# Optimization experiments

Measured on AMD Instinct MI355X. Metric: run time of the kernel, lower is better.

Reference implementation:

```python
import jax, jax.numpy as jnp
import numpy as np
from jax import lax

TAU = 20.0
DT = 1.0
THRESH = 1.0

# Hard-threshold spike with surrogate gradient (triangular window around thresh),
# matching torch SpikeFunction.
@jax.custom_vjp
def spike(v):
    return (v >= THRESH).astype(v.dtype)

def _spike_fwd(v):
    return spike(v), v

def _spike_bwd(v, g):
    return (g * jnp.clip(1.0 - jnp.abs(v - THRESH), 0.0, 1.0),)

spike.defvjp(_spike_fwd, _spike_bwd)


def setup_inputs() -> dict:
    key = jax.random.key(0)
    B, F, T = 64, 2048, 512
    x = jax.random.normal(key, (B, F, T), dtype=jnp.float32)
    return {"x": x}


def reference(x) -> jnp.ndarray:
    # x: [B, F, T]; sequential LIF membrane scan over T with spike + hard reset.
    B, F, T = x.shape

    def step(v, x_t):
        v = v + (x_t - v) * (DT / TAU)
        s = spike(v)
        v = v * (1.0 - s)  # reset-to-zero on spike
        return v, s

    x_tmajor = jnp.moveaxis(x, 2, 0)  # [T, B, F]
    v0 = jnp.zeros((B, F), dtype=x.dtype)
    _, spikes = lax.scan(step, v0, x_tmajor)  # spikes: [T, B, F]
    return jnp.moveaxis(spikes, 0, 2)  # [B, F, T]
```

## Files before the change

kernel.cpp:

```cpp
#include <hip/hip_runtime.h>


#define T_LEN 512
#define CHUNK 64
#define ROWS 256
#define NCHUNK (T_LEN / CHUNK)

__global__ __launch_bounds__(256, 2)
void lif_kernel(const float* __restrict__ x, float* __restrict__ out) {
    __shared__ float tile[CHUNK][ROWS];
    const int tid  = threadIdx.x;
    const int row0 = blockIdx.x * ROWS;
    const float k = 1.0f / 20.0f;
    float v = 0.0f;

    for (int ch = 0; ch < NCHUNK; ++ch) {
        const int t0 = ch * CHUNK;

        #pragma unroll
        for (int p = 0; p < 16; ++p) {
            const int q = p * 256 + tid;
            const int r = q >> 4;
            const int c = (q & 15) * 4;
            const float4 val = *reinterpret_cast<const float4*>(
                x + (size_t)(row0 + r) * T_LEN + t0 + c);
            tile[c + 0][r ^ (c + 0)] = val.x;
            tile[c + 1][r ^ (c + 1)] = val.y;
            tile[c + 2][r ^ (c + 2)] = val.z;
            tile[c + 3][r ^ (c + 3)] = val.w;
        }
        __syncthreads();

        #pragma unroll
        for (int t = 0; t < CHUNK; ++t) {
            const float xv = tile[t][tid ^ t];
            v = v + (xv - v) * k;
            const bool fire = (v >= 1.0f);
            tile[t][tid ^ t] = fire ? 1.0f : 0.0f;
            v = fire ? 0.0f : v;
        }
        __syncthreads();

        #pragma unroll
        for (int p = 0; p < 16; ++p) {
            const int q = p * 256 + tid;
            const int r = q >> 4;
            const int c = (q & 15) * 4;
            float4 val;
            val.x = tile[c + 0][r ^ (c + 0)];
            val.y = tile[c + 1][r ^ (c + 1)];
            val.z = tile[c + 2][r ^ (c + 2)];
            val.w = tile[c + 3][r ^ (c + 3)];
            *reinterpret_cast<float4*>(
                out + (size_t)(row0 + r) * T_LEN + t0 + c) = val;
        }
        __syncthreads();
    }
}

extern "C" void kernel_launch(void* const* d_in, const int* in_sizes, int n_in,
                              void* d_out, int out_size, void* d_ws, size_t ws_size,
                              hipStream_t stream) {
    const float* x = (const float*)d_in[0];
    float* out = (float*)d_out;
    const int rows = in_sizes[0] / T_LEN;
    const int grid = rows / ROWS;
    lif_kernel<<<dim3(grid), dim3(ROWS), 0, stream>>>(x, out);
}
```

Before: 441.2 us.

## Use single-wavefront blocks with register double-buffered prefetch of next chunk

Shrinks each block to one 64-lane wavefront handling 64 rows, so the __syncthreads barriers are replaced by LDS waitcnt fences. The next chunk's global loads are issued into a 16-entry float4 register buffer before the current chunk's sequential scan runs, overlapping memory latency with compute. This raises register pressure and quadruples the grid size, and it relies on wavefront-synchronous LDS semantics for correctness.

```diff
diff --git a/kernel.cpp b/kernel.cpp
--- a/kernel.cpp
+++ b/kernel.cpp
@@ -3,58 +3,75 @@
 
 #define T_LEN 512
 #define CHUNK 64
-#define ROWS 256
 #define NCHUNK (T_LEN / CHUNK)
 
-__global__ __launch_bounds__(256, 2)
+__global__ __launch_bounds__(64, 2)
 void lif_kernel(const float* __restrict__ x, float* __restrict__ out) {
-    __shared__ float tile[CHUNK][ROWS];
-    const int tid  = threadIdx.x;
-    const int row0 = blockIdx.x * ROWS;
-    const float k = 1.0f / 20.0f;
+    __shared__ float tile[CHUNK][64];
+    const int lane = threadIdx.x;
+    const size_t row0 = (size_t)blockIdx.x * 64;
+    const float kk = 1.0f / 20.0f;
     float v = 0.0f;
 
+    const float* xb = x + row0 * T_LEN;
+    float* ob = out + row0 * T_LEN;
+
+    const int rL = lane >> 4;
+    const int cL = (lane & 15) * 4;
+
+    float4 buf[16];
+
+    #pragma unroll
+    for (int p = 0; p < 16; ++p) {
+        const int r = p * 4 + rL;
+        buf[p] = *reinterpret_cast<const float4*>(xb + (size_t)r * T_LEN + cL);
+    }
+
     for (int ch = 0; ch < NCHUNK; ++ch) {
-        const int t0 = ch * CHUNK;
-
         #pragma unroll
         for (int p = 0; p < 16; ++p) {
-            const int q = p * 256 + tid;
-            const int r = q >> 4;
-            const int c = (q & 15) * 4;
-            const float4 val = *reinterpret_cast<const float4*>(
-                x + (size_t)(row0 + r) * T_LEN + t0 + c);
-            tile[c + 0][r ^ (c + 0)] = val.x;
-            tile[c + 1][r ^ (c + 1)] = val.y;
-            tile[c + 2][r ^ (c + 2)] = val.z;
-            tile[c + 3][r ^ (c + 3)] = val.w;
+            const int r = p * 4 + rL;
+            tile[cL + 0][r ^ (cL + 0)] = buf[p].x;
+            tile[cL + 1][r ^ (cL + 1)] = buf[p].y;
+            tile[cL + 2][r ^ (cL + 2)] = buf[p].z;
+            tile[cL + 3][r ^ (cL + 3)] = buf[p].w;
         }
-        __syncthreads();
+
+        if (ch + 1 < NCHUNK) {
+            const float* xc = xb + (size_t)(ch + 1) * CHUNK;
+            #pragma unroll
+            for (int p = 0; p < 16; ++p) {
+                const int r = p * 4 + rL;
+                buf[p] = *reinterpret_cast<const float4*>(xc + (size_t)r * T_LEN + cL);
+            }
+        }
+
+        asm volatile("s_waitcnt lgkmcnt(0)" ::: "memory");
 
         #pragma unroll
         for (int t = 0; t < CHUNK; ++t) {
-            const float xv = tile[t][tid ^ t];
-            v = v + (xv - v) * k;
+            const float xv = tile[t][lane ^ t];
+            v = v + (xv - v) * kk;
             const bool fire = (v >= 1.0f);
-            tile[t][tid ^ t] = fire ? 1.0f : 0.0f;
+            tile[t][lane ^ t] = fire ? 1.0f : 0.0f;
             v = fire ? 0.0f : v;
         }
-        __syncthreads();
 
+        asm volatile("s_waitcnt lgkmcnt(0)" ::: "memory");
+
+        float* oc = ob + (size_t)ch * CHUNK;
         #pragma unroll
         for (int p = 0; p < 16; ++p) {
-            const int q = p * 256 + tid;
-            const int r = q >> 4;
-            const int c = (q & 15) * 4;
-            float4 val;
-            val.x = tile[c + 0][r ^ (c + 0)];
-            val.y = tile[c + 1][r ^ (c + 1)];
-            val.z = tile[c + 2][r ^ (c + 2)];
-            val.w = tile[c + 3][r ^ (c + 3)];
-            *reinterpret_cast<float4*>(
-                out + (size_t)(row0 + r) * T_LEN + t0 + c) = val;
+            const int r = p * 4 + rL;
+            float4 s;
+            s.x = tile[cL + 0][r ^ (cL + 0)];
+            s.y = tile[cL + 1][r ^ (cL + 1)];
+            s.z = tile[cL + 2][r ^ (cL + 2)];
+            s.w = tile[cL + 3][r ^ (cL + 3)];
+            *reinterpret_cast<float4*>(oc + (size_t)r * T_LEN + cL) = s;
         }
-        __syncthreads();
+
+        asm volatile("s_waitcnt lgkmcnt(0)" ::: "memory");
     }
 }
 
@@ -64,6 +81,6 @@
     const float* x = (const float*)d_in[0];
     float* out = (float*)d_out;
     const int rows = in_sizes[0] / T_LEN;
-    const int grid = rows / ROWS;
-    lif_kernel<<<dim3(grid), dim3(ROWS), 0, stream>>>(x, out);
+    const int grid = rows / 64;
+    lif_kernel<<<dim3(grid), dim3(64), 0, stream>>>(x, out);
 }
```

Measured after the change: 441.9 us. Within noise of the previous version (+0.2%).

## Replace tiled sequential LIF scan with wave-level parallel prefix and spike-free fast path

Applied to the files above, without the earlier changes.

Each wave handles one row at a time. Each lane holds 8 contiguous timesteps, and the no-reset membrane trajectory is computed with a shuffle-based parallel prefix scan using precomputed decay powers. If no lane's membrane comes near threshold (checked with a ballot against a 0.95 margin), the row is written as zeros directly. Otherwise every lane reruns the exact sequential scan for that row. This drops the shared-memory transpose and the barriers and streams memory more directly, but rows that do spike pay a costly redundant serial fallback.

```diff
diff --git a/kernel.cpp b/kernel.cpp
--- a/kernel.cpp
+++ b/kernel.cpp
@@ -1,60 +1,82 @@
 #include <hip/hip_runtime.h>
 
 
+typedef float f8 __attribute__((ext_vector_type(8)));
+
 #define T_LEN 512
-#define CHUNK 64
-#define ROWS 256
-#define NCHUNK (T_LEN / CHUNK)
+#define ROWS_PER_WAVE 16
+#define WAVES_PER_BLOCK 4
 
-__global__ __launch_bounds__(256, 2)
+__global__ __launch_bounds__(256, 8)
 void lif_kernel(const float* __restrict__ x, float* __restrict__ out) {
-    __shared__ float tile[CHUNK][ROWS];
-    const int tid  = threadIdx.x;
-    const int row0 = blockIdx.x * ROWS;
-    const float k = 1.0f / 20.0f;
-    float v = 0.0f;
+    constexpr float  K  = 1.0f / 20.0f;
+    constexpr double Kd = (double)(1.0f / 20.0f);
+    constexpr double A1 = 1.0 - Kd;
+    constexpr double A2 = A1 * A1;
+    constexpr double A4 = A2 * A2;
+    constexpr double A8 = A4 * A4;
+    constexpr double A16 = A8 * A8;
+    constexpr double A32 = A16 * A16;
+    constexpr double A64 = A32 * A32;
+    constexpr double A128 = A64 * A64;
+    constexpr double A256 = A128 * A128;
+    constexpr float C[6] = {(float)A8,  (float)A16,  (float)A32,
+                            (float)A64, (float)A128, (float)A256};
 
-    for (int ch = 0; ch < NCHUNK; ++ch) {
-        const int t0 = ch * CHUNK;
+    const int lane = threadIdx.x & 63;
+    const int wid  = blockIdx.x * WAVES_PER_BLOCK + (threadIdx.x >> 6);
+    const size_t row0 = (size_t)wid * ROWS_PER_WAVE;
+
+    const f8 zero8 = {0.f, 0.f, 0.f, 0.f, 0.f, 0.f, 0.f, 0.f};
+
+    f8 xv = *(const f8*)(x + row0 * T_LEN + lane * 8);
+
+    for (int rr = 0; rr < ROWS_PER_WAVE; ++rr) {
+        const size_t base = (row0 + rr) * T_LEN;
+        const f8 xc = xv;
+        if (rr + 1 < ROWS_PER_WAVE)
+            xv = *(const f8*)(x + base + T_LEN + lane * 8);
+
+        float b = 0.0f;
+        #pragma unroll
+        for (int j = 0; j < 8; ++j) b = b + (xc[j] - b) * K;
 
         #pragma unroll
-        for (int p = 0; p < 16; ++p) {
-            const int q = p * 256 + tid;
-            const int r = q >> 4;
-            const int c = (q & 15) * 4;
-            const float4 val = *reinterpret_cast<const float4*>(
-                x + (size_t)(row0 + r) * T_LEN + t0 + c);
-            tile[c + 0][r ^ (c + 0)] = val.x;
-            tile[c + 1][r ^ (c + 1)] = val.y;
-            tile[c + 2][r ^ (c + 2)] = val.z;
-            tile[c + 3][r ^ (c + 3)] = val.w;
+        for (int s = 0; s < 6; ++s) {
+            const float o = __shfl_up(b, 1 << s);
+            const float f = fmaf(o, C[s], b);
+            b = (lane >= (1 << s)) ? f : b;
         }
-        __syncthreads();
+        float u = __shfl_up(b, 1);
+        u = (lane == 0) ? 0.0f : u;
 
+        float v = u;
+        float mx = -1.0f;
         #pragma unroll
-        for (int t = 0; t < CHUNK; ++t) {
-            const float xv = tile[t][tid ^ t];
-            v = v + (xv - v) * k;
-            const bool fire = (v >= 1.0f);
-            tile[t][tid ^ t] = fire ? 1.0f : 0.0f;
-            v = fire ? 0.0f : v;
+        for (int j = 0; j < 8; ++j) {
+            v = v + (xc[j] - v) * K;
+            mx = fmaxf(mx, v);
         }
-        __syncthreads();
 
-        #pragma unroll
-        for (int p = 0; p < 16; ++p) {
-            const int q = p * 256 + tid;
-            const int r = q >> 4;
-            const int c = (q & 15) * 4;
-            float4 val;
-            val.x = tile[c + 0][r ^ (c + 0)];
-            val.y = tile[c + 1][r ^ (c + 1)];
-            val.z = tile[c + 2][r ^ (c + 2)];
-            val.w = tile[c + 3][r ^ (c + 3)];
-            *reinterpret_cast<float4*>(
-                out + (size_t)(row0 + r) * T_LEN + t0 + c) = val;
+        if (__builtin_expect(__ballot(mx >= 0.95f) != 0, 0)) {
+            const float* xr = x + base;
+            unsigned m = 0;
+            float vv = 0.0f;
+            for (int t = 0; t < T_LEN; ++t) {
+                const float xt = xr[t];
+                vv = vv + (xt - vv) * K;
+                const bool fire = (vv >= 1.0f);
+                if (fire) vv = 0.0f;
+                if (fire && ((t >> 3) == lane)) m |= (1u << (t & 7));
+            }
+            f8 s8;
+            #pragma unroll
+            for (int j = 0; j < 8; ++j)
+                s8[j] = ((m >> j) & 1u) ? 1.0f : 0.0f;
+            *(f8*)(out + base + lane * 8) = s8;
+        } else {
+            *(f8*)(out + base + lane * 8) = zero8;
         }
-        __syncthreads();
     }
 }
 
@@ -64,6 +86,6 @@
     const float* x = (const float*)d_in[0];
     float* out = (float*)d_out;
     const int rows = in_sizes[0] / T_LEN;
-    const int grid = rows / ROWS;
-    lif_kernel<<<dim3(grid), dim3(ROWS), 0, stream>>>(x, out);
+    const int grid = rows / (ROWS_PER_WAVE * WAVES_PER_BLOCK);
+    lif_kernel<<<dim3(grid), dim3(64 * WAVES_PER_BLOCK), 0, stream>>>(x, out);
 }
```

Result: faster. 430.0 us (-2.5%).
